# Optimization experiments

Hardware: AMD Instinct MI355X
Metric: run time of the kernel (lower is better)

## Reference

```python
import jax, jax.numpy as jnp
import numpy as np

N = 100000
E = 3200000
D = 128


def setup_inputs() -> dict:
    key = jax.random.key(0)
    k1, k2, k3, k4 = jax.random.split(key, 4)
    x = jax.random.normal(k1, (N, D), dtype=jnp.float32)
    edge_index = jax.random.randint(k2, (2, E), 0, N, dtype=jnp.int64)
    W1 = jax.random.normal(k3, (D, 16), dtype=jnp.float32) * (1.0 / np.sqrt(D))
    b1 = jnp.zeros((16,), dtype=jnp.float32)
    W2 = jax.random.normal(k4, (16, 2), dtype=jnp.float32) * (1.0 / np.sqrt(16))
    b2 = jnp.zeros((2,), dtype=jnp.float32)
    return {"x": x, "edge_index": edge_index, "W1": W1, "b1": b1, "W2": W2, "b2": b2}


def _gcn_conv(h, src, dst, norm, W, b):
    # transform first (out_dim <= in_dim), then normalized scatter-add aggregation
    h = h @ W                                   # [N, out]
    msg = h[src] * norm[:, None]                # [E+N, out] gathered messages
    agg = jax.ops.segment_sum(msg, dst, num_segments=N)
    return agg + b


def reference(x, edge_index, W1, b1, W2, b2):
    loops = jnp.arange(N, dtype=edge_index.dtype)
    src = jnp.concatenate([edge_index[0], loops])   # row (message source)
    dst = jnp.concatenate([edge_index[1], loops])   # col (aggregation target)
    # symmetric GCN normalization: deg over dst, norm = d^-1/2[src] * d^-1/2[dst]
    deg = jax.ops.segment_sum(jnp.ones_like(src, dtype=x.dtype), dst, num_segments=N)
    dinv = jnp.where(deg > 0, jax.lax.rsqrt(deg), 0.0)
    norm = dinv[src] * dinv[dst]

    h = _gcn_conv(x, src, dst, norm, W1, b1)
    h = jax.nn.relu(h)
    h = _gcn_conv(h, src, dst, norm, W2, b2)
    return jax.nn.log_softmax(h, axis=1)
```

## Files before the change

### kernel.cpp

```cpp
#include <hip/hip_runtime.h>
#include <hip/hip_fp16.h>
#include <math.h>

#define N_NODES 100000
#define N_EDGES 3200000
#define D_IN    128
#define H1      16

#define BSH     8
#define NPB     256
#define NB      391
#define CAP     13056
#define PBLK    512
#define CHUNK   6250
#define ELS_CAP 12128
#define NLINES  (ELS_CAP / 16)
#define MROWS   64


__global__ __launch_bounds__(512) void k_partition(const int* __restrict__ ei,
                                                   int* __restrict__ cursor,
                                                   unsigned int* __restrict__ eop) {
    __shared__ int h[512];
    __shared__ int loff[512];
    __shared__ int resv[NB];
    __shared__ unsigned short owner[NLINES];
    __shared__ unsigned char rank8[CHUNK];
    __shared__ unsigned int els[ELS_CAP];
    int t = threadIdx.x;
    h[t] = 0;
    __syncthreads();
    int c0 = blockIdx.x * CHUNK;
    const int* srcs = ei + c0;
    const int* dsts = ei + N_EDGES + c0;
    for (int i = t; i < CHUNK; i += 512)
        rank8[i] = (unsigned char)atomicAdd(&h[dsts[i] >> BSH], 1);
    __syncthreads();
    int cp = (h[t] + 15) & ~15;
    loff[t] = cp;
    __syncthreads();
    for (int o = 1; o < 512; o <<= 1) {
        int u = (t >= o) ? loff[t - o] : 0;
        __syncthreads();
        loff[t] += u;
        __syncthreads();
    }
    int inc = loff[t];
    int totalpad = loff[511];
    int ex = inc - cp;
    __syncthreads();
    loff[t] = ex;
    if (t < NB && cp) {
        resv[t] = atomicAdd(&cursor[t], cp);
        int l0 = ex >> 4;
        for (int k = 0; k < (cp >> 4); ++k) owner[l0 + k] = (unsigned short)t;
    }
    for (int i = t; i < totalpad; i += 512) els[i] = 0xFFFFFFFFu;
    __syncthreads();
    for (int i = t; i < CHUNK; i += 512) {
        int s = srcs[i];
        int d = dsts[i];
        int b = d >> BSH;
        els[loff[b] + (int)rank8[i]] = ((unsigned)s << BSH) | (unsigned)(d & (NPB - 1));
    }
    __syncthreads();
    for (int i = t; i < totalpad; i += 512) {
        int b   = owner[i >> 4];
        int pos = resv[b] + (i - loff[b]);
        if (pos < CAP)
            eop[(size_t)b * CAP + pos] = els[i];
    }
}

__global__ __launch_bounds__(512) void k_build(const int* __restrict__ cursor,
                                               unsigned int* __restrict__ eop,
                                               int* __restrict__ nstart,
                                               int* __restrict__ ndeg,
                                               float* __restrict__ dinv) {
    __shared__ unsigned int els[CAP];
    __shared__ int cnt[NPB];
    __shared__ int off[NPB];
    int t = threadIdx.x, b = blockIdx.x;
    if (t < NPB) cnt[t] = 0;
    __syncthreads();
    int n = cursor[b]; if (n > CAP) n = CAP;
    unsigned int* reg = eop + (size_t)b * CAP;
    for (int i4 = t; i4 < (n >> 2); i4 += 512) {
        uint4 w = ((const uint4*)reg)[i4];
        unsigned int e0 = w.x, e1 = w.y, e2 = w.z, e3 = w.w;
        int r;
        if ((int)e0 >= 0) { r = atomicAdd(&cnt[e0 & (NPB - 1)], 1); e0 |= (unsigned)r << 25; }
        if ((int)e1 >= 0) { r = atomicAdd(&cnt[e1 & (NPB - 1)], 1); e1 |= (unsigned)r << 25; }
        if ((int)e2 >= 0) { r = atomicAdd(&cnt[e2 & (NPB - 1)], 1); e2 |= (unsigned)r << 25; }
        if ((int)e3 >= 0) { r = atomicAdd(&cnt[e3 & (NPB - 1)], 1); e3 |= (unsigned)r << 25; }
        ((uint4*)els)[i4] = make_uint4(e0, e1, e2, e3);
    }
    __syncthreads();
    int val = (t < NPB) ? cnt[t] : 0;
    if (t < NPB) off[t] = val;
    __syncthreads();
    for (int o = 1; o < NPB; o <<= 1) {
        int u = 0;
        if (t < NPB && t >= o) u = off[t - o];
        __syncthreads();
        if (t < NPB) off[t] += u;
        __syncthreads();
    }
    if (t < NPB) {
        int ex = off[t] - val;
        off[t] = ex;
        int node = (b << BSH) + t;
        if (node < N_NODES) {
            nstart[node] = b * CAP + ex;
            ndeg[node]   = val;
            dinv[node]   = rsqrtf((float)(val + 1));
        }
    }
    __syncthreads();
    for (int i4 = t; i4 < (n >> 2); i4 += 512) {
        uint4 w = ((const uint4*)els)[i4];
        unsigned int e; unsigned s;
        e = w.x; s = (e >> 8) & 0x1FFFFu;
        if (s < N_NODES) reg[off[e & (NPB - 1)] + (int)(e >> 25)] = s;
        e = w.y; s = (e >> 8) & 0x1FFFFu;
        if (s < N_NODES) reg[off[e & (NPB - 1)] + (int)(e >> 25)] = s;
        e = w.z; s = (e >> 8) & 0x1FFFFu;
        if (s < N_NODES) reg[off[e & (NPB - 1)] + (int)(e >> 25)] = s;
        e = w.w; s = (e >> 8) & 0x1FFFFu;
        if (s < N_NODES) reg[off[e & (NPB - 1)] + (int)(e >> 25)] = s;
    }
}

__global__ __launch_bounds__(256) void k_mm1(const float* __restrict__ x,
                                             const float* __restrict__ W1,
                                             const float* __restrict__ dinv,
                                             __half* __restrict__ h1h) {
    __shared__ float sX[MROWS][D_IN + 1];
    int t = threadIdx.x;
    int r0 = blockIdx.x * MROWS;
    for (int i = t; i < MROWS * (D_IN / 4); i += 256) {
        int row = i >> 5, c4 = i & 31;
        int grow = r0 + row;
        float4 v = (grow < N_NODES) ? ((const float4*)x)[(size_t)grow * 32 + c4]
                                    : make_float4(0.f, 0.f, 0.f, 0.f);
        sX[row][c4 * 4 + 0] = v.x; sX[row][c4 * 4 + 1] = v.y;
        sX[row][c4 * 4 + 2] = v.z; sX[row][c4 * 4 + 3] = v.w;
    }
    __syncthreads();
    int lane = t & 63;
    int c0 = __builtin_amdgcn_readfirstlane((t >> 6) * 4);
    float a0 = 0.f, a1 = 0.f, a2 = 0.f, a3 = 0.f;
#pragma unroll 4
    for (int d = 0; d < D_IN; ++d) {
        float xv = sX[lane][d];
        a0 = fmaf(xv, W1[d * 16 + c0 + 0], a0);
        a1 = fmaf(xv, W1[d * 16 + c0 + 1], a1);
        a2 = fmaf(xv, W1[d * 16 + c0 + 2], a2);
        a3 = fmaf(xv, W1[d * 16 + c0 + 3], a3);
    }
    int grow = r0 + lane;
    if (grow < N_NODES) {
        float di = dinv[grow];
        __half2* o = (__half2*)(h1h + (size_t)grow * H1 + c0);
        o[0] = __floats2half2_rn(a0 * di, a1 * di);
        o[1] = __floats2half2_rn(a2 * di, a3 * di);
    }
}

__global__ __launch_bounds__(256) void k_agg1(const unsigned int* __restrict__ eop,
                                              const int* __restrict__ nstart,
                                              const int* __restrict__ ndeg,
                                              const __half* __restrict__ h1h,
                                              const float* __restrict__ dinv,
                                              const float* __restrict__ b1,
                                              const float* __restrict__ W2,
                                              float2* __restrict__ h2f) {
    int t = threadIdx.x;
    int g = t >> 4, l = t & 15;
    int node = blockIdx.x * 16 + g;
    int e0 = nstart[node], e1 = e0 + ndeg[node];
    float acc = 0.f;
    int j = e0;
    for (; j + 4 <= e1; j += 4) {
        int s0 = eop[j], s1 = eop[j + 1], s2 = eop[j + 2], s3 = eop[j + 3];
        acc += __half2float(h1h[s0 * H1 + l]) + __half2float(h1h[s1 * H1 + l])
             + __half2float(h1h[s2 * H1 + l]) + __half2float(h1h[s3 * H1 + l]);
    }
    for (; j < e1; ++j) acc += __half2float(h1h[(int)eop[j] * H1 + l]);
    float di = dinv[node];
    float s  = acc + __half2float(h1h[node * H1 + l]);
    float h  = fmaxf(fmaf(di, s, b1[l]), 0.f);
    float p0 = h * W2[2 * l], p1 = h * W2[2 * l + 1];
#pragma unroll
    for (int off = 1; off < 16; off <<= 1) {
        p0 += __shfl_xor(p0, off);
        p1 += __shfl_xor(p1, off);
    }
    if (l == 0) h2f[node] = make_float2(p0 * di, p1 * di);
}

__global__ __launch_bounds__(256) void k_agg2(const unsigned int* __restrict__ eop,
                                              const int* __restrict__ nstart,
                                              const int* __restrict__ ndeg,
                                              const float2* __restrict__ h2f,
                                              const float* __restrict__ dinv,
                                              const float* __restrict__ b2,
                                              float* __restrict__ out) {
    int tg = blockIdx.x * 256 + threadIdx.x;
    int node = tg >> 2, l = tg & 3;
    if (node >= N_NODES) return;
    int e0 = nstart[node], e1 = e0 + ndeg[node];
    float ax = 0.f, ay = 0.f;
    for (int j = e0 + l; j < e1; j += 4) {
        float2 m = h2f[eop[j]];
        ax += m.x; ay += m.y;
    }
    ax += __shfl_xor(ax, 1); ay += __shfl_xor(ay, 1);
    ax += __shfl_xor(ax, 2); ay += __shfl_xor(ay, 2);
    if (l == 0) {
        float di = dinv[node];
        float2 self = h2f[node];
        float a0 = fmaf(di, ax + self.x, b2[0]);
        float a1 = fmaf(di, ay + self.y, b2[1]);
        float m  = fmaxf(a0, a1);
        float lg = logf(expf(a0 - m) + expf(a1 - m));
        out[2 * node]     = a0 - m - lg;
        out[2 * node + 1] = a1 - m - lg;
    }
}

extern "C" void kernel_launch(void* const* d_in, const int* in_sizes, int n_in,
                              void* d_out, int out_size, void* d_ws, size_t ws_size,
                              hipStream_t stream) {
    const float* x  = (const float*)d_in[0];
    const int*   ei = (const int*)d_in[1];
    const float* W1 = (const float*)d_in[2];
    const float* b1 = (const float*)d_in[3];
    const float* W2 = (const float*)d_in[4];
    const float* b2 = (const float*)d_in[5];
    float* out = (float*)d_out;

    int*          cursor = (int*)d_ws;
    int*          nstart = cursor + 512;
    int*          ndeg   = nstart + 100352;
    float*        dinv   = (float*)(ndeg + 100352);
    __half*       h1h    = (__half*)(dinv + 100352);
    float2*       h2f    = (float2*)(h1h + (size_t)100352 * H1);
    unsigned int* eop    = (unsigned int*)(h2f + 100352);

    hipMemsetAsync(cursor, 0, 512 * sizeof(int), stream);
    k_partition<<<PBLK, 512, 0, stream>>>(ei, cursor, eop);
    k_build    <<<NB,   512, 0, stream>>>(cursor, eop, nstart, ndeg, dinv);
    k_mm1      <<<(N_NODES + MROWS - 1) / MROWS, 256, 0, stream>>>(x, W1, dinv, h1h);
    k_agg1     <<<N_NODES / 16, 256, 0, stream>>>(eop, nstart, ndeg, h1h, dinv, b1, W2, h2f);
    k_agg2     <<<(N_NODES * 4 + 255) / 256, 256, 0, stream>>>(eop, nstart, ndeg, h2f, dinv, b2, out);
}
```

Before: 221.6 us.

## Use wave-shuffle scans, int2 edge loads, and half2 cooperative gathers in agg1

Replaces the shared-memory Hillis-Steele prefix scans in the partition and build kernels with wavefront shuffle scans plus a small cross-wave combine, which cuts the number of barriers. The partition kernel now reads edge indices as int2 pairs. The first aggregation kernel gives each node 8 lanes instead of 16, has each lane gather a half2, loads 8 neighbor indices cooperatively and broadcasts them with shuffles, and handles the tail with masking. Together these aim to reduce synchronization and per-edge index-load overhead, in exchange for more shuffle instructions and masked wasted loads on the tail.

New measurement: 206.4 us. 6.8% less time.

```diff
diff --git a/kernel.cpp b/kernel.cpp
--- a/kernel.cpp
+++ b/kernel.cpp
@@ -24,6 +24,7 @@
     __shared__ int h[512];
     __shared__ int loff[512];
     __shared__ int resv[NB];
+    __shared__ int wsum[8], wpre[8];
     __shared__ unsigned short owner[NLINES];
     __shared__ unsigned char rank8[CHUNK];
     __shared__ unsigned int els[ELS_CAP];
@@ -31,24 +32,37 @@
     h[t] = 0;
     __syncthreads();
     int c0 = blockIdx.x * CHUNK;
-    const int* srcs = ei + c0;
-    const int* dsts = ei + N_EDGES + c0;
-    for (int i = t; i < CHUNK; i += 512)
-        rank8[i] = (unsigned char)atomicAdd(&h[dsts[i] >> BSH], 1);
+    const int2* s2 = (const int2*)(ei + c0);
+    const int2* d2 = (const int2*)(ei + N_EDGES + c0);
+    for (int i = t; i < CHUNK / 2; i += 512) {
+        int2 dd = d2[i];
+        rank8[2 * i]     = (unsigned char)atomicAdd(&h[dd.x >> BSH], 1);
+        rank8[2 * i + 1] = (unsigned char)atomicAdd(&h[dd.y >> BSH], 1);
+    }
     __syncthreads();
     int cp = (h[t] + 15) & ~15;
-    loff[t] = cp;
-    __syncthreads();
-    for (int o = 1; o < 512; o <<= 1) {
-        int u = (t >= o) ? loff[t - o] : 0;
-        __syncthreads();
-        loff[t] += u;
-        __syncthreads();
-    }
-    int inc = loff[t];
-    int totalpad = loff[511];
+    int lane = t & 63, w = t >> 6;
+    int v = cp;
+#pragma unroll
+    for (int o = 1; o < 64; o <<= 1) {
+        int u = __shfl_up(v, o);
+        if (lane >= o) v += u;
+    }
+    if (lane == 63) wsum[w] = v;
+    __syncthreads();
+    if (t < 8) {
+        int s = wsum[t];
+#pragma unroll
+        for (int o = 1; o < 8; o <<= 1) {
+            int u = __shfl_up(s, o);
+            if (t >= o) s += u;
+        }
+        wpre[t] = s;
+    }
+    __syncthreads();
+    int inc = v + ((w > 0) ? wpre[w - 1] : 0);
+    int totalpad = wpre[7];
     int ex = inc - cp;
-    __syncthreads();
     loff[t] = ex;
     if (t < NB && cp) {
         resv[t] = atomicAdd(&cursor[t], cp);
@@ -57,11 +71,13 @@
     }
     for (int i = t; i < totalpad; i += 512) els[i] = 0xFFFFFFFFu;
     __syncthreads();
-    for (int i = t; i < CHUNK; i += 512) {
-        int s = srcs[i];
-        int d = dsts[i];
-        int b = d >> BSH;
-        els[loff[b] + (int)rank8[i]] = ((unsigned)s << BSH) | (unsigned)(d & (NPB - 1));
+    for (int i = t; i < CHUNK / 2; i += 512) {
+        int2 ss = s2[i];
+        int2 dd = d2[i];
+        els[loff[dd.x >> BSH] + (int)rank8[2 * i]] =
+            ((unsigned)ss.x << BSH) | (unsigned)(dd.x & (NPB - 1));
+        els[loff[dd.y >> BSH] + (int)rank8[2 * i + 1]] =
+            ((unsigned)ss.y << BSH) | (unsigned)(dd.y & (NPB - 1));
     }
     __syncthreads();
     for (int i = t; i < totalpad; i += 512) {
@@ -80,14 +96,15 @@
     __shared__ unsigned int els[CAP];
     __shared__ int cnt[NPB];
     __shared__ int off[NPB];
+    __shared__ int wsum[4], wpre[4];
     int t = threadIdx.x, b = blockIdx.x;
     if (t < NPB) cnt[t] = 0;
     __syncthreads();
     int n = cursor[b]; if (n > CAP) n = CAP;
     unsigned int* reg = eop + (size_t)b * CAP;
     for (int i4 = t; i4 < (n >> 2); i4 += 512) {
-        uint4 w = ((const uint4*)reg)[i4];
-        unsigned int e0 = w.x, e1 = w.y, e2 = w.z, e3 = w.w;
+        uint4 wv = ((const uint4*)reg)[i4];
+        unsigned int e0 = wv.x, e1 = wv.y, e2 = wv.z, e3 = wv.w;
         int r;
         if ((int)e0 >= 0) { r = atomicAdd(&cnt[e0 & (NPB - 1)], 1); e0 |= (unsigned)r << 25; }
         if ((int)e1 >= 0) { r = atomicAdd(&cnt[e1 & (NPB - 1)], 1); e1 |= (unsigned)r << 25; }
@@ -97,17 +114,28 @@
     }
     __syncthreads();
     int val = (t < NPB) ? cnt[t] : 0;
-    if (t < NPB) off[t] = val;
-    __syncthreads();
-    for (int o = 1; o < NPB; o <<= 1) {
-        int u = 0;
-        if (t < NPB && t >= o) u = off[t - o];
-        __syncthreads();
-        if (t < NPB) off[t] += u;
-        __syncthreads();
-    }
+    int lane = t & 63, w = t >> 6;
+    int v = val;
+#pragma unroll
+    for (int o = 1; o < 64; o <<= 1) {
+        int u = __shfl_up(v, o);
+        if (lane >= o) v += u;
+    }
+    if (lane == 63 && w < 4) wsum[w] = v;
+    __syncthreads();
+    if (t < 4) {
+        int s = wsum[t];
+#pragma unroll
+        for (int o = 1; o < 4; o <<= 1) {
+            int u = __shfl_up(s, o);
+            if (t >= o) s += u;
+        }
+        wpre[t] = s;
+    }
+    __syncthreads();
     if (t < NPB) {
-        int ex = off[t] - val;
+        int inc = v + ((w > 0) ? wpre[w - 1] : 0);
+        int ex = inc - val;
         off[t] = ex;
         int node = (b << BSH) + t;
         if (node < N_NODES) {
@@ -118,15 +146,15 @@
     }
     __syncthreads();
     for (int i4 = t; i4 < (n >> 2); i4 += 512) {
-        uint4 w = ((const uint4*)els)[i4];
+        uint4 wv = ((const uint4*)els)[i4];
         unsigned int e; unsigned s;
-        e = w.x; s = (e >> 8) & 0x1FFFFu;
+        e = wv.x; s = (e >> 8) & 0x1FFFFu;
         if (s < N_NODES) reg[off[e & (NPB - 1)] + (int)(e >> 25)] = s;
-        e = w.y; s = (e >> 8) & 0x1FFFFu;
+        e = wv.y; s = (e >> 8) & 0x1FFFFu;
         if (s < N_NODES) reg[off[e & (NPB - 1)] + (int)(e >> 25)] = s;
-        e = w.z; s = (e >> 8) & 0x1FFFFu;
+        e = wv.z; s = (e >> 8) & 0x1FFFFu;
         if (s < N_NODES) reg[off[e & (NPB - 1)] + (int)(e >> 25)] = s;
-        e = w.w; s = (e >> 8) & 0x1FFFFu;
+        e = wv.w; s = (e >> 8) & 0x1FFFFu;
         if (s < N_NODES) reg[off[e & (NPB - 1)] + (int)(e >> 25)] = s;
     }
 }
@@ -176,23 +204,46 @@
                                               const float* __restrict__ W2,
                                               float2* __restrict__ h2f) {
     int t = threadIdx.x;
-    int g = t >> 4, l = t & 15;
-    int node = blockIdx.x * 16 + g;
-    int e0 = nstart[node], e1 = e0 + ndeg[node];
-    float acc = 0.f;
+    int g = t >> 3, l = t & 7;
+    int base = (t & 63) & ~7;
+    int node = blockIdx.x * 32 + g;
+    int e0 = nstart[node], deg = ndeg[node];
+    const __half2* H = (const __half2*)h1h;
+    float a0 = 0.f, a1 = 0.f;
+    int nfull = deg & ~7;
     int j = e0;
-    for (; j + 4 <= e1; j += 4) {
-        int s0 = eop[j], s1 = eop[j + 1], s2 = eop[j + 2], s3 = eop[j + 3];
-        acc += __half2float(h1h[s0 * H1 + l]) + __half2float(h1h[s1 * H1 + l])
-             + __half2float(h1h[s2 * H1 + l]) + __half2float(h1h[s3 * H1 + l]);
-    }
-    for (; j < e1; ++j) acc += __half2float(h1h[(int)eop[j] * H1 + l]);
+    for (; j < e0 + nfull; j += 8) {
+        int s = (int)eop[j + l];
+#pragma unroll
+        for (int k = 0; k < 8; ++k) {
+            int sk = __shfl(s, base + k);
+            float2 f = __half22float2(H[sk * 8 + l]);
+            a0 += f.x; a1 += f.y;
+        }
+    }
+    int r = e0 + deg - j;
+    if (r) {
+        int s = (l < r) ? (int)eop[j + l] : -1;
+#pragma unroll
+        for (int k = 0; k < 8; ++k) {
+            int sk = __shfl(s, base + k);
+            int su = (sk >= 0) ? sk : 0;
+            float m = (sk >= 0) ? 1.f : 0.f;
+            float2 f = __half22float2(H[su * 8 + l]);
+            a0 = fmaf(f.x, m, a0); a1 = fmaf(f.y, m, a1);
+        }
+    }
     float di = dinv[node];
-    float s  = acc + __half2float(h1h[node * H1 + l]);
-    float h  = fmaxf(fmaf(di, s, b1[l]), 0.f);
-    float p0 = h * W2[2 * l], p1 = h * W2[2 * l + 1];
-#pragma unroll
-    for (int off = 1; off < 16; off <<= 1) {
+    float2 self = __half22float2(H[node * 8 + l]);
+    float s0 = a0 + self.x, s1 = a1 + self.y;
+    float2 bb = ((const float2*)b1)[l];
+    float h0 = fmaxf(fmaf(di, s0, bb.x), 0.f);
+    float h1v = fmaxf(fmaf(di, s1, bb.y), 0.f);
+    float4 wv = ((const float4*)W2)[l];
+    float p0 = h0 * wv.x + h1v * wv.z;
+    float p1 = h0 * wv.y + h1v * wv.w;
+#pragma unroll
+    for (int off = 1; off < 8; off <<= 1) {
         p0 += __shfl_xor(p0, off);
         p1 += __shfl_xor(p1, off);
     }
@@ -252,6 +303,6 @@
     k_partition<<<PBLK, 512, 0, stream>>>(ei, cursor, eop);
     k_build    <<<NB,   512, 0, stream>>>(cursor, eop, nstart, ndeg, dinv);
     k_mm1      <<<(N_NODES + MROWS - 1) / MROWS, 256, 0, stream>>>(x, W1, dinv, h1h);
-    k_agg1     <<<N_NODES / 16, 256, 0, stream>>>(eop, nstart, ndeg, h1h, dinv, b1, W2, h2f);
+    k_agg1     <<<N_NODES / 32, 256, 0, stream>>>(eop, nstart, ndeg, h1h, dinv, b1, W2, h2f);
     k_agg2     <<<(N_NODES * 4 + 255) / 256, 256, 0, stream>>>(eop, nstart, ndeg, h2f, dinv, b2, out);
 }
```
